# Performance work log

Hardware: AMD Instinct MI355X
Metric: run time of the kernel (lower is better)

Reference implementation:

```python
import jax, jax.numpy as jnp
import numpy as np

N_STATIONS = 276
CONTEXT_LEN = 384  # args.context_len * 2
TARGET_LEN = 96
BATCH = 4096


def setup_inputs() -> dict:
    key = jax.random.key(0)
    k1, k2, k3, k4, k5, k6 = jax.random.split(key, 6)
    z = jax.random.normal(k1, (BATCH, CONTEXT_LEN), dtype=jnp.float32)
    stations = jax.random.randint(k2, (BATCH,), 0, N_STATIONS, dtype=jnp.int64)
    # per-station Linear params (nn.Linear(context_len, target_len) x n_stations)
    lim = 1.0 / np.sqrt(CONTEXT_LEN)
    W = jax.random.uniform(k3, (N_STATIONS, TARGET_LEN, CONTEXT_LEN), jnp.float32, -lim, lim)
    b = jax.random.uniform(k4, (N_STATIONS, TARGET_LEN), jnp.float32, -lim, lim)
    loc = jax.random.normal(k5, (N_STATIONS,), dtype=jnp.float32)
    scale = jax.random.uniform(k6, (N_STATIONS,), jnp.float32, 0.5, 2.0)
    return {"z": z, "stations": stations, "W": W, "b": b, "loc": loc, "scale": scale}


def reference(z, stations, W, b, loc, scale):
    # norm: (z - loc[i]) / scale[i]
    loc_i = loc[stations][:, None]      # (bs, 1)
    scale_i = scale[stations][:, None]  # (bs, 1)
    zn = (z - loc_i) / scale_i          # (bs, context_len)
    # per-sample station-specific Linear: batched GEMV via gathered weights
    out = jnp.einsum("boi,bi->bo", W[stations], zn) + b[stations]  # (bs, target_len)
    # denorm then softplus
    out = out * scale_i + loc_i
    return jax.nn.softplus(out)
```

## Files before the change

kernel.cpp:

```cpp
#include <hip/hip_runtime.h>
#include <hip/hip_bf16.h>
#include <math.h>

#define N_STATIONS 276
#define CTX 384
#define TGT 96
#define BATCH 4096
#define NTILE_N 6
#define KSPLIT 2
#define KHALF 192
#define NSTEP 6
#define NTASK (N_STATIONS * NTILE_N * KSPLIT)
#define CPX2 (NTASK / 8)

typedef __attribute__((ext_vector_type(8))) short bf16x8;
typedef __attribute__((ext_vector_type(4))) float f32x4;

__device__ __forceinline__ short f2bf(float f) {
    return (short)__builtin_bit_cast(unsigned short, __float2bfloat16(f));
}
__device__ __forceinline__ float bf2f(short h) {
    unsigned u = ((unsigned)(unsigned short)h) << 16;
    return __builtin_bit_cast(float, u);
}
__device__ __forceinline__ void cvt_hilo(float4 a, float4 b, bf16x8& hi, bf16x8& lo) {
    float f[8] = {a.x, a.y, a.z, a.w, b.x, b.y, b.z, b.w};
#pragma unroll
    for (int i = 0; i < 8; ++i) {
        short h = f2bf(f[i]);
        hi[i] = h;
        lo[i] = f2bf(f[i] - bf2f(h));
    }
}
__device__ __forceinline__ bf16x8 cvt_norm(float4 a, float4 b, float inv, float nb) {
    float f[8] = {a.x, a.y, a.z, a.w, b.x, b.y, b.z, b.w};
    bf16x8 r;
#pragma unroll
    for (int i = 0; i < 8; ++i) r[i] = f2bf(fmaf(f[i], inv, nb));
    return r;
}

__global__ __launch_bounds__(1024) void build_lists(
    const int* __restrict__ stations,
    int* __restrict__ order,
    int* __restrict__ offsets)
{
    __shared__ int cnt[N_STATIONS];
    __shared__ int cnt2[N_STATIONS];
    __shared__ int poff[N_STATIONS + 1];
    const int tid = threadIdx.x;
    for (int i = tid; i < N_STATIONS; i += 1024) { cnt[i] = 0; cnt2[i] = 0; }
    __syncthreads();
    for (int b = tid; b < BATCH; b += 1024) atomicAdd(&cnt[stations[b]], 1);
    __syncthreads();
    if (tid < 64) {
        int run = 0;
        for (int base = 0; base < N_STATIONS; base += 64) {
            const int i = base + tid;
            int v = (i < N_STATIONS) ? cnt[i] : 0;
#pragma unroll
            for (int off = 1; off < 64; off <<= 1) {
                int u = __shfl_up(v, off, 64);
                if (tid >= off) v += u;
            }
            if (i < N_STATIONS) poff[i + 1] = run + v;
            run += __shfl(v, 63, 64);
        }
        if (tid == 0) poff[0] = 0;
    }
    __syncthreads();
    for (int b = tid; b < BATCH; b += 1024) {
        int s = stations[b];
        int p = atomicAdd(&cnt2[s], 1);
        order[poff[s] + p] = b;
    }
    if (tid <= N_STATIONS) offsets[tid] = poff[tid];
}

__global__ __launch_bounds__(64, 1) void nlinear_splitk(
    const float* __restrict__ z,
    const int*   __restrict__ order,
    const int*   __restrict__ offsets,
    const float* __restrict__ W,
    const float* __restrict__ loc,
    const float* __restrict__ scale,
    float*       __restrict__ out)
{
    const int bid0 = blockIdx.x;
    const int bid  = (bid0 & 7) * CPX2 + (bid0 >> 3);
    const int half = bid & 1;
    const int task = bid >> 1;
    const int s    = task / NTILE_N;
    const int n0   = (task - s * NTILE_N) * 16;

    const int start = offsets[s];
    const int m     = offsets[s + 1] - start;
    if (m == 0) return;

    const int l  = threadIdx.x;
    const int lr = l & 15;
    const int kh = (l >> 4) * 8;

    const float lc  = loc[s];
    const float inv = 1.0f / scale[s];
    const float nb  = -lc * inv;

    const float* wrow = W + ((size_t)s * TGT + n0 + lr) * CTX + half * KHALF + kh;
    bf16x8 bhi[NSTEP], blo[NSTEP];
#pragma unroll
    for (int kk = 0; kk < NSTEP; ++kk) {
        float4 w0 = *reinterpret_cast<const float4*>(wrow + kk * 32);
        float4 w1 = *reinterpret_cast<const float4*>(wrow + kk * 32 + 4);
        cvt_hilo(w0, w1, bhi[kk], blo[kk]);
    }

    const int ntiles = (m + 15) >> 4;
    const int rbase  = (l >> 4) * 4;

    for (int t = 0; t < ntiles; ++t) {
        int j = t * 16 + lr; if (j > m - 1) j = m - 1;
        const float* zr = z + (size_t)order[start + j] * CTX + half * KHALF + kh;

        f32x4 acc = {0.f, 0.f, 0.f, 0.f};
#pragma unroll
        for (int kk = 0; kk < NSTEP; ++kk) {
            float4 a0 = *reinterpret_cast<const float4*>(zr + kk * 32);
            float4 a1 = *reinterpret_cast<const float4*>(zr + kk * 32 + 4);
            bf16x8 af = cvt_norm(a0, a1, inv, nb);
            acc = __builtin_amdgcn_mfma_f32_16x16x32_bf16(af, bhi[kk], acc, 0, 0, 0);
            acc = __builtin_amdgcn_mfma_f32_16x16x32_bf16(af, blo[kk], acc, 0, 0, 0);
        }
#pragma unroll
        for (int r = 0; r < 4; ++r) {
            const int jj = t * 16 + rbase + r;
            if (jj < m) {
                const int oid = order[start + jj];
                atomicAdd(&out[(size_t)oid * TGT + n0 + lr], acc[r]);
            }
        }
    }
}

__global__ __launch_bounds__(256) void epilogue(
    const int*   __restrict__ stations,
    const float* __restrict__ bias,
    const float* __restrict__ loc,
    const float* __restrict__ scale,
    float*       __restrict__ out)
{
    const int gid = blockIdx.x * 256 + threadIdx.x;
    if (gid >= BATCH * TGT) return;
    const int id = gid / TGT;
    const int c  = gid - id * TGT;
    const int s  = stations[id];
    float v = (out[gid] + bias[(size_t)s * TGT + c]) * scale[s] + loc[s];
    out[gid] = fmaxf(v, 0.f) + log1pf(expf(-fabsf(v)));
}

extern "C" void kernel_launch(void* const* d_in, const int* in_sizes, int n_in,
                              void* d_out, int out_size, void* d_ws, size_t ws_size,
                              hipStream_t stream) {
    const float* z        = (const float*)d_in[0];
    const int*   stations = (const int*)  d_in[1];
    const float* W        = (const float*)d_in[2];
    const float* bias     = (const float*)d_in[3];
    const float* loc      = (const float*)d_in[4];
    const float* scale    = (const float*)d_in[5];
    float* out = (float*)d_out;

    int* order   = (int*)d_ws;
    int* offsets = order + BATCH;

    hipMemsetAsync(out, 0, (size_t)BATCH * TGT * sizeof(float), stream);
    build_lists<<<1, 1024, 0, stream>>>(stations, order, offsets);
    nlinear_splitk<<<NTASK, 64, 0, stream>>>(z, order, offsets, W, loc, scale, out);
    epilogue<<<(BATCH * TGT + 255) / 256, 256, 0, stream>>>(stations, bias, loc, scale, out);
}
```

Measured before the change: 33.99 us.

## Compute all output columns per block and fuse bias/softplus epilogue, dropping atomics

Replaces the split-K, per-column-tile decomposition with blocks that each own a station and a strided subset of 16-row tiles, computing all 96 outputs over the full 384-long K. This removes the memset, the atomic accumulation and the separate epilogue kernel, applying bias, denorm and softplus directly in registers. In exchange, weights are re-read from global/L2 and re-converted to hi/lo bf16 for every row tile rather than kept in registers, and there are fewer blocks (276*4 versus 276*12). Many of those blocks exit early because stations average about 15 rows.

Measured after the change: 58.40 us. 1.72x slower.

```diff
diff --git a/kernel.cpp b/kernel.cpp
--- a/kernel.cpp
+++ b/kernel.cpp
@@ -6,12 +6,9 @@
 #define CTX 384
 #define TGT 96
 #define BATCH 4096
-#define NTILE_N 6
-#define KSPLIT 2
-#define KHALF 192
-#define NSTEP 6
-#define NTASK (N_STATIONS * NTILE_N * KSPLIT)
-#define CPX2 (NTASK / 8)
+#define NSLOT 4
+#define NBLK (N_STATIONS * NSLOT)
+#define CPX (NBLK / 8)
 
 typedef __attribute__((ext_vector_type(8))) short bf16x8;
 typedef __attribute__((ext_vector_type(4))) float f32x4;
@@ -77,84 +74,80 @@
     if (tid <= N_STATIONS) offsets[tid] = poff[tid];
 }
 
-__global__ __launch_bounds__(64, 1) void nlinear_splitk(
+__global__ __launch_bounds__(64, 1) void nlinear_allcols(
     const float* __restrict__ z,
     const int*   __restrict__ order,
     const int*   __restrict__ offsets,
     const float* __restrict__ W,
+    const float* __restrict__ bias,
     const float* __restrict__ loc,
     const float* __restrict__ scale,
     float*       __restrict__ out)
 {
     const int bid0 = blockIdx.x;
-    const int bid  = (bid0 & 7) * CPX2 + (bid0 >> 3);
-    const int half = bid & 1;
-    const int task = bid >> 1;
-    const int s    = task / NTILE_N;
-    const int n0   = (task - s * NTILE_N) * 16;
+    const int bid  = (bid0 & 7) * CPX + (bid0 >> 3);
+    const int s    = bid >> 2;
+    const int t0   = bid & 3;
 
     const int start = offsets[s];
     const int m     = offsets[s + 1] - start;
-    if (m == 0) return;
+    if (t0 * 16 >= m) return;
 
     const int l  = threadIdx.x;
     const int lr = l & 15;
     const int kh = (l >> 4) * 8;
 
     const float lc  = loc[s];
-    const float inv = 1.0f / scale[s];
+    const float sc  = scale[s];
+    const float inv = 1.0f / sc;
     const float nb  = -lc * inv;
 
-    const float* wrow = W + ((size_t)s * TGT + n0 + lr) * CTX + half * KHALF + kh;
-    bf16x8 bhi[NSTEP], blo[NSTEP];
+    const float* wbase = W + (size_t)s * TGT * CTX;
+    const int    rbase = (l >> 4) * 4;
+
+    for (int t = t0; t * 16 < m; t += NSLOT) {
+        int j = t * 16 + lr; if (j > m - 1) j = m - 1;
+        const float* zr = z + (size_t)order[start + j] * CTX + kh;
+        bf16x8 af[12];
 #pragma unroll
-    for (int kk = 0; kk < NSTEP; ++kk) {
-        float4 w0 = *reinterpret_cast<const float4*>(wrow + kk * 32);
-        float4 w1 = *reinterpret_cast<const float4*>(wrow + kk * 32 + 4);
-        cvt_hilo(w0, w1, bhi[kk], blo[kk]);
-    }
-
-    const int ntiles = (m + 15) >> 4;
-    const int rbase  = (l >> 4) * 4;
-
-    for (int t = 0; t < ntiles; ++t) {
-        int j = t * 16 + lr; if (j > m - 1) j = m - 1;
-        const float* zr = z + (size_t)order[start + j] * CTX + half * KHALF + kh;
-
-        f32x4 acc = {0.f, 0.f, 0.f, 0.f};
-#pragma unroll
-        for (int kk = 0; kk < NSTEP; ++kk) {
+        for (int kk = 0; kk < 12; ++kk) {
             float4 a0 = *reinterpret_cast<const float4*>(zr + kk * 32);
             float4 a1 = *reinterpret_cast<const float4*>(zr + kk * 32 + 4);
-            bf16x8 af = cvt_norm(a0, a1, inv, nb);
-            acc = __builtin_amdgcn_mfma_f32_16x16x32_bf16(af, bhi[kk], acc, 0, 0, 0);
-            acc = __builtin_amdgcn_mfma_f32_16x16x32_bf16(af, blo[kk], acc, 0, 0, 0);
+            af[kk] = cvt_norm(a0, a1, inv, nb);
         }
+
+        int oid[4]; bool ok[4];
 #pragma unroll
         for (int r = 0; r < 4; ++r) {
             const int jj = t * 16 + rbase + r;
-            if (jj < m) {
-                const int oid = order[start + jj];
-                atomicAdd(&out[(size_t)oid * TGT + n0 + lr], acc[r]);
+            ok[r]  = (jj < m);
+            oid[r] = order[start + (ok[r] ? jj : 0)];
+        }
+
+        for (int nt = 0; nt < 6; ++nt) {
+            const float* wrow = wbase + ((size_t)nt * 16 + lr) * CTX + kh;
+            f32x4 ah = {0.f, 0.f, 0.f, 0.f};
+            f32x4 al = {0.f, 0.f, 0.f, 0.f};
+#pragma unroll
+            for (int kk = 0; kk < 12; ++kk) {
+                float4 w0 = *reinterpret_cast<const float4*>(wrow + kk * 32);
+                float4 w1 = *reinterpret_cast<const float4*>(wrow + kk * 32 + 4);
+                bf16x8 bhi, blo;
+                cvt_hilo(w0, w1, bhi, blo);
+                ah = __builtin_amdgcn_mfma_f32_16x16x32_bf16(af[kk], bhi, ah, 0, 0, 0);
+                al = __builtin_amdgcn_mfma_f32_16x16x32_bf16(af[kk], blo, al, 0, 0, 0);
+            }
+            const float bv = bias[(size_t)s * TGT + nt * 16 + lr];
+#pragma unroll
+            for (int r = 0; r < 4; ++r) {
+                if (ok[r]) {
+                    float v = (ah[r] + al[r] + bv) * sc + lc;
+                    out[(size_t)oid[r] * TGT + nt * 16 + lr] =
+                        fmaxf(v, 0.f) + log1pf(expf(-fabsf(v)));
+                }
             }
         }
     }
-}
-
-__global__ __launch_bounds__(256) void epilogue(
-    const int*   __restrict__ stations,
-    const float* __restrict__ bias,
-    const float* __restrict__ loc,
-    const float* __restrict__ scale,
-    float*       __restrict__ out)
-{
-    const int gid = blockIdx.x * 256 + threadIdx.x;
-    if (gid >= BATCH * TGT) return;
-    const int id = gid / TGT;
-    const int c  = gid - id * TGT;
-    const int s  = stations[id];
-    float v = (out[gid] + bias[(size_t)s * TGT + c]) * scale[s] + loc[s];
-    out[gid] = fmaxf(v, 0.f) + log1pf(expf(-fabsf(v)));
 }
 
 extern "C" void kernel_launch(void* const* d_in, const int* in_sizes, int n_in,
@@ -171,8 +164,6 @@
     int* order   = (int*)d_ws;
     int* offsets = order + BATCH;
 
-    hipMemsetAsync(out, 0, (size_t)BATCH * TGT * sizeof(float), stream);
     build_lists<<<1, 1024, 0, stream>>>(stations, order, offsets);
-    nlinear_splitk<<<NTASK, 64, 0, stream>>>(z, order, offsets, W, loc, scale, out);
-    epilogue<<<(BATCH * TGT + 255) / 256, 256, 0, stream>>>(stations, bias, loc, scale, out);
+    nlinear_allcols<<<NBLK, 64, 0, stream>>>(z, order, offsets, W, bias, loc, scale, out);
 }
```
